# Kernel tuning notes

Measured on AMD Instinct MI355X. Metric: run time of the kernel, lower is better.

The kernel has to match this reference:

```python
import jax, jax.numpy as jnp
import numpy as np
from jax import lax

B, C, W = 16, 64, 125000  # batch, EEG channels, raw samples
KH, KW, SW, OC = 3, 2500, 1250, 32


def setup_inputs() -> dict:
    key = jax.random.key(0)
    ks = jax.random.split(key, 10)
    inp = {
        "x": jax.random.normal(ks[0], (B, 1, C, W), dtype=jnp.float32),
        # Conv2d(1->32, kernel=(3,2500))
        "conv_w": jax.random.normal(ks[1], (OC, 1, KH, KW), dtype=jnp.float32) * 0.02,
        "conv_b": jax.random.normal(ks[2], (OC,), dtype=jnp.float32) * 0.02,
        # Conv2d(32->1, kernel=(1,1))
        "conv2_w": jax.random.normal(ks[3], (1, OC, 1, 1), dtype=jnp.float32) * 0.1,
        "conv2_b": jax.random.normal(ks[4], (1,), dtype=jnp.float32) * 0.1,
        # nn.RNN(input_size=1, hidden_size=1): scalar weights
        "w_ih": jax.random.normal(ks[5], (1, 1), dtype=jnp.float32),
        "w_hh": jax.random.normal(ks[6], (1, 1), dtype=jnp.float32),
        "b_ih": jax.random.normal(ks[7], (1,), dtype=jnp.float32) * 0.1,
        "b_hh": jax.random.normal(ks[8], (1,), dtype=jnp.float32) * 0.1,
        # torch.rand(num_layers=1, B, 1) hidden init, reused for every row i
        "h0": jax.random.uniform(ks[9], (1, B, 1), dtype=jnp.float32),
    }
    return inp


def reference(x, conv_w, conv_b, conv2_w, conv2_b, w_ih, w_hh, b_ih, b_hh, h0):
    # F.pad(x, (0,0,1,1), 'replicate'): pad channel (height) dim by 1 each side
    xp = jnp.pad(x, ((0, 0), (0, 0), (1, 1), (0, 0)), mode="edge")
    # conv + relu -> [B, 32, C, T]
    y = lax.conv_general_dilated(
        xp, conv_w, window_strides=(1, SW), padding="VALID",
        dimension_numbers=("NCHW", "OIHW", "NCHW"))
    y = jax.nn.relu(y + conv_b[None, :, None, None])
    # 1x1 conv 32->1 + relu -> [B, C, T]
    z = jnp.einsum("bohw,o->bhw", y, conv2_w[0, :, 0, 0]) + conv2_b[0]
    z = jax.nn.relu(z)
    # Elman RNN with scalar weights, scanned over T; carry is [B, C]
    wih, whh = w_ih[0, 0], w_hh[0, 0]
    bias = b_ih[0] + b_hh[0]
    h_init = jnp.broadcast_to(h0[0, :, 0][:, None], z.shape[:2])  # [B, C]

    def step(h, xt):  # xt: [B, C]
        h = jnp.tanh(wih * xt + whh * h + bias)
        return h, None

    xs = jnp.moveaxis(z, -1, 0)  # [T, B, C]
    h_final, _ = lax.scan(step, h_init, xs)
    return jax.nn.sigmoid(h_final)  # [B, C]
```

## Files before the change

kernel.cpp:

```cpp
#include <hip/hip_runtime.h>
#include <math.h>

#define B_ 16
#define C_ 64
#define J_ 100
#define T_ 99
#define KW_ 1250
#define KP_ 1280
#define N_ 192
#define M_ (B_*C_*J_)
#define BM 128
#define BK 32
#define NCHUNK 40

typedef __attribute__((ext_vector_type(8))) _Float16 half8;
typedef __attribute__((ext_vector_type(4))) float f32x4;
typedef __attribute__((ext_vector_type(2), aligned(8))) float f32x2;

__global__ __launch_bounds__(256) void wconv_kernel(const float* __restrict__ cw,
                                                    _Float16* __restrict__ wh)
{
    int n = blockIdx.x;
    int o = n / 6, rem = n - o * 6, kh = rem >> 1, hf = rem & 1;
    const float* src = cw + o * 7500 + kh * 2500 + hf * 1250;
    for (int k = threadIdx.x; k < KP_; k += 256)
        wh[n * KP_ + k] = (k < KW_) ? (_Float16)src[k] : (_Float16)0.f;
}

__global__ __launch_bounds__(256, 3) void gemm_kernel(const float* __restrict__ x,
                                                      const _Float16* __restrict__ wh,
                                                      _Float16* __restrict__ P)
{
    __shared__ __align__(16) _Float16 smA[2][BM * BK];

    const int tid  = threadIdx.x;
    const int bm0  = blockIdx.x * BM;
    const int lane = tid & 63;
    const int wave = tid >> 6;
    const int wm   = (wave & 1) * 64;
    const int wn   = (wave >> 1) * 96;
    const int l15  = lane & 15;
    const int lq   = lane >> 4;

    const float* ap[2]; int koff[2]; int adst[2];
#pragma unroll
    for (int u = 0; u < 2; u++) {
        int q  = u * 256 + tid;
        int rl = q >> 2, p = q & 3;
        int gr = bm0 + rl;
        int b  = gr / 6400;
        int j  = (gr - b * 6400) >> 6;
        int c  = gr & 63;
        long xrow = (long)(b * 64 + c) * 100 + j;
        ap[u]   = x + xrow * KW_ + p * 8;
        koff[u] = p * 8;
        adst[u] = q * 8;
    }
    const _Float16* bbase = wh + (size_t)(wn + l15) * KP_ + lq * 8;

    f32x4 acc[4][6];
#pragma unroll
    for (int mi = 0; mi < 4; mi++)
#pragma unroll
        for (int ni = 0; ni < 6; ni++) acc[mi][ni] = (f32x4){0.f, 0.f, 0.f, 0.f};

    f32x2 areg[2][4];
#define LOADA(k0)                                                              \
    do {                                                                       \
        _Pragma("unroll") for (int u = 0; u < 2; u++)                          \
        _Pragma("unroll") for (int j2 = 0; j2 < 4; j2++) {                     \
            int k = (k0) + koff[u] + j2 * 2;           \
            areg[u][j2] = (k + 2 <= KW_)                                       \
                ? *(const f32x2*)(ap[u] + (k0) + j2 * 2)                       \
                : (f32x2){0.f, 0.f};                                           \
        }                                                                      \
    } while (0)

    LOADA(0);

    for (int ck = 0; ck < NCHUNK; ck++) {
        const int slot = ck & 1;
        _Float16* Ab = &smA[slot][0];

        half8 bcur = *(const half8*)(bbase + (size_t)ck * BK);

#pragma unroll
        for (int u = 0; u < 2; u++) {
            half8 h;
#pragma unroll
            for (int j2 = 0; j2 < 4; j2++) {
                h[2 * j2]     = (_Float16)areg[u][j2].x;
                h[2 * j2 + 1] = (_Float16)areg[u][j2].y;
            }
            *(half8*)(Ab + adst[u]) = h;
        }

        asm volatile("s_waitcnt lgkmcnt(0)" ::: "memory");
        __builtin_amdgcn_s_barrier();
        __builtin_amdgcn_sched_barrier(0);

        if (ck + 1 < NCHUNK) LOADA((ck + 1) * BK);

        half8 afr[4];
#pragma unroll
        for (int mi = 0; mi < 4; mi++)
            afr[mi] = *(const half8*)(Ab + (wm + mi * 16 + l15) * BK + lq * 8);

#pragma unroll
        for (int ni = 0; ni < 6; ni++) {
            half8 bnext = bcur;
            if (ni < 5)
                bnext = *(const half8*)(bbase + (size_t)(ni + 1) * 16 * KP_
                                              + (size_t)ck * BK);
#pragma unroll
            for (int mi = 0; mi < 4; mi++)
                acc[mi][ni] = __builtin_amdgcn_mfma_f32_16x16x32_f16(
                    afr[mi], bcur, acc[mi][ni], 0, 0, 0);
            bcur = bnext;
        }
    }

#pragma unroll
    for (int mi = 0; mi < 4; mi++) {
        int mrow = bm0 + wm + mi * 16 + lq * 4;
#pragma unroll
        for (int ni = 0; ni < 6; ni++) {
            int n = wn + ni * 16 + l15;
#pragma unroll
            for (int r2 = 0; r2 < 4; r2++)
                P[(size_t)(mrow + r2) * N_ + n] = (_Float16)acc[mi][ni][r2];
        }
    }
#undef LOADA
}

__global__ __launch_bounds__(256) void combine_kernel(const _Float16* __restrict__ P,
                                                      const float* __restrict__ conv_b,
                                                      const float* __restrict__ c2w,
                                                      const float* __restrict__ c2b,
                                                      float* __restrict__ z)
{
    __shared__ float Pl[64][193];
    __shared__ float red[4][64];
    const int t   = blockIdx.x;
    const int b   = blockIdx.y;
    const int tid = threadIdx.x;
    const int c   = tid & 63;
    const int og  = tid >> 6;

    float v[8];
#pragma unroll
    for (int o = 0; o < 8; o++) v[o] = conv_b[og * 8 + o];

    for (int hf = 0; hf < 2; hf++) {
        const int j = t + hf;
        const _Float16* Pb = P + (size_t)((b * 100 + j) * 64) * N_;
        __syncthreads();
#pragma unroll
        for (int i = 0; i < 6; i++) {
            int e   = i * 256 + tid;
            half8 h = *(const half8*)(Pb + e * 8);
            int row = e / 24;
            int col = (e - row * 24) * 8;
#pragma unroll
            for (int u = 0; u < 8; u++) Pl[row][col + u] = (float)h[u];
        }
        __syncthreads();
#pragma unroll
        for (int kh = 0; kh < 3; kh++) {
            int r = c + kh - 1;
            r = r < 0 ? 0 : (r > 63 ? 63 : r);
#pragma unroll
            for (int o = 0; o < 8; o++)
                v[o] += Pl[r][(og * 8 + o) * 6 + kh * 2 + hf];
        }
    }

    float part = 0.f;
#pragma unroll
    for (int o = 0; o < 8; o++) part += fmaxf(v[o], 0.f) * c2w[og * 8 + o];
    red[og][c] = part;
    __syncthreads();
    if (og == 0) {
        float zz = red[0][c] + red[1][c] + red[2][c] + red[3][c] + c2b[0];
        z[t * (B_ * C_) + b * 64 + c] = fmaxf(zz, 0.f);
    }
}

__global__ __launch_bounds__(256) void rnn_kernel(const float* __restrict__ z,
                                                  const float* __restrict__ w_ih,
                                                  const float* __restrict__ w_hh,
                                                  const float* __restrict__ b_ih,
                                                  const float* __restrict__ b_hh,
                                                  const float* __restrict__ h0,
                                                  float* __restrict__ out)
{
    __shared__ float zs[50][256];
    const int tid = threadIdx.x;
    const int g   = blockIdx.x * 256 + tid;
    const int b   = g >> 6;
    const float wih  = w_ih[0];
    const float whh  = w_hh[0];
    const float bias = b_ih[0] + b_hh[0];
    float h = h0[b];
    for (int t0 = 0; t0 < T_; t0 += 50) {
        const int nt = (T_ - t0) < 50 ? (T_ - t0) : 50;
        __syncthreads();
        for (int tt = 0; tt < nt; tt++)
            zs[tt][tid] = z[(t0 + tt) * (B_ * C_) + g];
        __syncthreads();
        for (int tt = 0; tt < nt; tt++)
            h = tanhf(fmaf(wih, zs[tt][tid], fmaf(whh, h, bias)));
    }
    out[g] = 1.f / (1.f + expf(-h));
}

extern "C" void kernel_launch(void* const* d_in, const int* in_sizes, int n_in,
                              void* d_out, int out_size, void* d_ws, size_t ws_size,
                              hipStream_t stream)
{
    const float* x   = (const float*)d_in[0];
    const float* cw  = (const float*)d_in[1];
    const float* cb  = (const float*)d_in[2];
    const float* c2w = (const float*)d_in[3];
    const float* c2b = (const float*)d_in[4];
    const float* wih = (const float*)d_in[5];
    const float* whh = (const float*)d_in[6];
    const float* bih = (const float*)d_in[7];
    const float* bhh = (const float*)d_in[8];
    const float* h0  = (const float*)d_in[9];
    float* out = (float*)d_out;

    const size_t whbytes = (size_t)N_ * KP_ * sizeof(_Float16);
    const size_t pbytes  = (size_t)M_ * N_ * sizeof(_Float16);
    const size_t zbytes  = (size_t)B_ * C_ * T_ * sizeof(float);

    if (ws_size < whbytes + pbytes + zbytes) return;

    _Float16* wh = (_Float16*)d_ws;
    _Float16* P  = (_Float16*)((char*)d_ws + whbytes);
    float*    z  = (float*)((char*)d_ws + whbytes + pbytes);

    wconv_kernel<<<N_, 256, 0, stream>>>(cw, wh);
    gemm_kernel<<<M_ / BM, 256, 0, stream>>>(x, wh, P);
    combine_kernel<<<dim3(T_, B_), 256, 0, stream>>>(P, cb, c2w, c2b, z);
    rnn_kernel<<<4, 256, 0, stream>>>(z, wih, whh, bih, bhh, h0, out);
}
```

Before: 860.0 us.

## Pre-pack A to fp16 tiles and stage GEMM via async global-to-LDS loads

Adds a pack kernel that converts the input x to fp16 and writes it in a chunk-tiled layout. The GEMM then streams A and B tiles into a triple-buffered LDS with global_load_lds and vmcnt-based waits, instead of converting floats in registers and reading B straight from global memory. The goal is to overlap memory with MFMA work and remove in-loop conversions and strided B loads. In exchange there is an extra pass over x (read fp32, write fp16 workspace), more LDS use per block, and occupancy lowered to 2.

New measurement: 841.5 us. 2.1% less time.

```diff
diff --git a/kernel.cpp b/kernel.cpp
--- a/kernel.cpp
+++ b/kernel.cpp
@@ -3,19 +3,23 @@
 
 #define B_ 16
 #define C_ 64
-#define J_ 100
 #define T_ 99
 #define KW_ 1250
 #define KP_ 1280
 #define N_ 192
-#define M_ (B_*C_*J_)
+#define M_ (B_*C_*100)
 #define BM 128
 #define BK 32
 #define NCHUNK 40
 
 typedef __attribute__((ext_vector_type(8))) _Float16 half8;
+typedef __attribute__((ext_vector_type(2))) _Float16 half2_t;
 typedef __attribute__((ext_vector_type(4))) float f32x4;
 typedef __attribute__((ext_vector_type(2), aligned(8))) float f32x2;
+
+#define GLD_LDS16(gp, lp) \
+    __builtin_amdgcn_global_load_lds((const __attribute__((address_space(1))) void*)(gp), \
+                                     (__attribute__((address_space(3))) void*)(lp), 16, 0, 0)
 
 __global__ __launch_bounds__(256) void wconv_kernel(const float* __restrict__ cw,
                                                     _Float16* __restrict__ wh)
@@ -27,36 +31,73 @@
         wh[n * KP_ + k] = (k < KW_) ? (_Float16)src[k] : (_Float16)0.f;
 }
 
-__global__ __launch_bounds__(256, 3) void gemm_kernel(const float* __restrict__ x,
+__global__ __launch_bounds__(256) void pack_kernel(const float* __restrict__ x,
+                                                   _Float16* __restrict__ Apk)
+{
+    __shared__ _Float16 As[16][1288];
+    const int g   = blockIdx.x;
+    const int tid = threadIdx.x;
+    const int i   = tid >> 4;
+    const int s   = tid & 15;
+    const int mrow = g * 16 + i;
+    const int b  = mrow / 6400;
+    const int jc = mrow - b * 6400;
+    const int j  = jc >> 6;
+    const int c  = jc & 63;
+    const float* xr = x + ((size_t)(b * 64 + c) * 100 + j) * KW_;
+
+#pragma unroll
+    for (int sw = 0; sw < 40; sw++) {
+        int t = s * 2 + sw * 32;
+        f32x2 v = (t + 2 <= KW_) ? *(const f32x2*)(xr + t) : (f32x2){0.f, 0.f};
+        *(half2_t*)(&As[i][t]) = (half2_t){(_Float16)v.x, (_Float16)v.y};
+    }
+    __syncthreads();
+
+    const int tile = g >> 3, ro = g & 7;
+#pragma unroll
+    for (int w = 0; w < 10; w++) {
+        int p  = tid + 256 * w;
+        int ck = p >> 6, rem = p & 63, ri = rem >> 2, kq = rem & 3;
+        half8 h = *(const half8*)(&As[ri][ck * 32 + kq * 8]);
+        *(half8*)(Apk + ((size_t)(tile * NCHUNK + ck) * 128 + ro * 16 + ri) * 32
+                      + kq * 8) = h;
+    }
+}
+
+__global__ __launch_bounds__(256, 2) void gemm_kernel(const _Float16* __restrict__ Apk,
                                                       const _Float16* __restrict__ wh,
                                                       _Float16* __restrict__ P)
 {
-    __shared__ __align__(16) _Float16 smA[2][BM * BK];
+    __shared__ __align__(16) _Float16 smA[3][BM * BK];
+    __shared__ __align__(16) _Float16 smB[3][N_ * BK];
 
     const int tid  = threadIdx.x;
-    const int bm0  = blockIdx.x * BM;
+    const int bt   = blockIdx.x;
     const int lane = tid & 63;
     const int wave = tid >> 6;
+    const int wq   = wave * 64;
     const int wm   = (wave & 1) * 64;
     const int wn   = (wave >> 1) * 96;
     const int l15  = lane & 15;
     const int lq   = lane >> 4;
 
-    const float* ap[2]; int koff[2]; int adst[2];
-#pragma unroll
-    for (int u = 0; u < 2; u++) {
-        int q  = u * 256 + tid;
-        int rl = q >> 2, p = q & 3;
-        int gr = bm0 + rl;
-        int b  = gr / 6400;
-        int j  = (gr - b * 6400) >> 6;
-        int c  = gr & 63;
-        long xrow = (long)(b * 64 + c) * 100 + j;
-        ap[u]   = x + xrow * KW_ + p * 8;
-        koff[u] = p * 8;
-        adst[u] = q * 8;
-    }
-    const _Float16* bbase = wh + (size_t)(wn + l15) * KP_ + lq * 8;
+    const _Float16* bp[3];
+#pragma unroll
+    for (int s = 0; s < 3; s++) {
+        int q = wq + 256 * s + lane;
+        bp[s] = wh + (size_t)(q >> 2) * KP_ + (q & 3) * 8;
+    }
+    const _Float16* abase = Apk + ((size_t)(bt * NCHUNK) << 12);
+
+#define STAGE(ck_, buf_) do {                                                    \
+        const _Float16* As_ = abase + ((size_t)(ck_) << 12);                     \
+        GLD_LDS16(As_ + (wq) * 8 + lane * 8,       &smA[buf_][(wq) * 8]);        \
+        GLD_LDS16(As_ + (wq + 256) * 8 + lane * 8, &smA[buf_][(wq + 256) * 8]);  \
+        GLD_LDS16(bp[0] + (size_t)(ck_) * BK,      &smB[buf_][(wq) * 8]);        \
+        GLD_LDS16(bp[1] + (size_t)(ck_) * BK,      &smB[buf_][(wq + 256) * 8]);  \
+        GLD_LDS16(bp[2] + (size_t)(ck_) * BK,      &smB[buf_][(wq + 512) * 8]);  \
+    } while (0)
 
     f32x4 acc[4][6];
 #pragma unroll
@@ -64,62 +105,45 @@
 #pragma unroll
         for (int ni = 0; ni < 6; ni++) acc[mi][ni] = (f32x4){0.f, 0.f, 0.f, 0.f};
 
-    f32x2 areg[2][4];
-#define LOADA(k0)                                                              \
-    do {                                                                       \
-        _Pragma("unroll") for (int u = 0; u < 2; u++)                          \
-        _Pragma("unroll") for (int j2 = 0; j2 < 4; j2++) {                     \
-            int k = (k0) + koff[u] + j2 * 2;           \
-            areg[u][j2] = (k + 2 <= KW_)                                       \
-                ? *(const f32x2*)(ap[u] + (k0) + j2 * 2)                       \
-                : (f32x2){0.f, 0.f};                                           \
-        }                                                                      \
-    } while (0)
-
-    LOADA(0);
-
+    STAGE(0, 0);
+    STAGE(1, 1);
+
+    int bi = 0;
     for (int ck = 0; ck < NCHUNK; ck++) {
-        const int slot = ck & 1;
-        _Float16* Ab = &smA[slot][0];
-
-        half8 bcur = *(const half8*)(bbase + (size_t)ck * BK);
-
-#pragma unroll
-        for (int u = 0; u < 2; u++) {
-            half8 h;
-#pragma unroll
-            for (int j2 = 0; j2 < 4; j2++) {
-                h[2 * j2]     = (_Float16)areg[u][j2].x;
-                h[2 * j2 + 1] = (_Float16)areg[u][j2].y;
-            }
-            *(half8*)(Ab + adst[u]) = h;
-        }
-
-        asm volatile("s_waitcnt lgkmcnt(0)" ::: "memory");
+        if (ck + 1 < NCHUNK) {
+            asm volatile("s_waitcnt vmcnt(5)" ::: "memory");
+        } else {
+            asm volatile("s_waitcnt vmcnt(0)" ::: "memory");
+        }
         __builtin_amdgcn_s_barrier();
         __builtin_amdgcn_sched_barrier(0);
 
-        if (ck + 1 < NCHUNK) LOADA((ck + 1) * BK);
-
-        half8 afr[4];
+        if (ck + 2 < NCHUNK) {
+            int b2 = bi + 2; if (b2 >= 3) b2 -= 3;
+            STAGE(ck + 2, b2);
+        }
+
+        const _Float16* Ab = &smA[bi][0];
+        const _Float16* Bb = &smB[bi][0];
+        half8 afr[4], bfr[6];
 #pragma unroll
         for (int mi = 0; mi < 4; mi++)
             afr[mi] = *(const half8*)(Ab + (wm + mi * 16 + l15) * BK + lq * 8);
-
-#pragma unroll
-        for (int ni = 0; ni < 6; ni++) {
-            half8 bnext = bcur;
-            if (ni < 5)
-                bnext = *(const half8*)(bbase + (size_t)(ni + 1) * 16 * KP_
-                                              + (size_t)ck * BK);
-#pragma unroll
-            for (int mi = 0; mi < 4; mi++)
+#pragma unroll
+        for (int ni = 0; ni < 6; ni++)
+            bfr[ni] = *(const half8*)(Bb + (wn + ni * 16 + l15) * BK + lq * 8);
+#pragma unroll
+        for (int mi = 0; mi < 4; mi++)
+#pragma unroll
+            for (int ni = 0; ni < 6; ni++)
                 acc[mi][ni] = __builtin_amdgcn_mfma_f32_16x16x32_f16(
-                    afr[mi], bcur, acc[mi][ni], 0, 0, 0);
-            bcur = bnext;
-        }
-    }
-
+                    afr[mi], bfr[ni], acc[mi][ni], 0, 0, 0);
+
+        bi = (bi == 2) ? 0 : bi + 1;
+    }
+#undef STAGE
+
+    const int bm0 = bt * BM;
 #pragma unroll
     for (int mi = 0; mi < 4; mi++) {
         int mrow = bm0 + wm + mi * 16 + lq * 4;
@@ -131,7 +155,6 @@
                 P[(size_t)(mrow + r2) * N_ + n] = (_Float16)acc[mi][ni][r2];
         }
     }
-#undef LOADA
 }
 
 __global__ __launch_bounds__(256) void combine_kernel(const _Float16* __restrict__ P,
@@ -231,18 +254,21 @@
     const float* h0  = (const float*)d_in[9];
     float* out = (float*)d_out;
 
-    const size_t whbytes = (size_t)N_ * KP_ * sizeof(_Float16);
-    const size_t pbytes  = (size_t)M_ * N_ * sizeof(_Float16);
-    const size_t zbytes  = (size_t)B_ * C_ * T_ * sizeof(float);
-
-    if (ws_size < whbytes + pbytes + zbytes) return;
-
-    _Float16* wh = (_Float16*)d_ws;
-    _Float16* P  = (_Float16*)((char*)d_ws + whbytes);
-    float*    z  = (float*)((char*)d_ws + whbytes + pbytes);
+    const size_t whbytes  = (size_t)N_ * KP_ * sizeof(_Float16);
+    const size_t apkbytes = (size_t)(M_ / BM) * NCHUNK * 4096 * sizeof(_Float16);
+    const size_t pbytes   = (size_t)M_ * N_ * sizeof(_Float16);
+    const size_t zbytes   = (size_t)B_ * C_ * T_ * sizeof(float);
+
+    if (ws_size < whbytes + apkbytes + pbytes + zbytes) return;
+
+    _Float16* wh  = (_Float16*)d_ws;
+    _Float16* Apk = (_Float16*)((char*)d_ws + whbytes);
+    _Float16* P   = (_Float16*)((char*)d_ws + whbytes + apkbytes);
+    float*    z   = (float*)((char*)d_ws + whbytes + apkbytes + pbytes);
 
     wconv_kernel<<<N_, 256, 0, stream>>>(cw, wh);
-    gemm_kernel<<<M_ / BM, 256, 0, stream>>>(x, wh, P);
+    pack_kernel<<<M_ / 16, 256, 0, stream>>>(x, Apk);
+    gemm_kernel<<<M_ / BM, 256, 0, stream>>>(Apk, wh, P);
     combine_kernel<<<dim3(T_, B_), 256, 0, stream>>>(P, cb, c2w, c2b, z);
     rnn_kernel<<<4, 256, 0, stream>>>(z, wih, whh, bih, bhh, h0, out);
 }
```

## Restructure GEMM A-tile staging into 128-wide K superchunks with coalesced row loads

Applied to the files above, without the earlier changes.

The GEMM now stages four BK chunks of the A operand at once. Each half-wave loads 16 full rows, with 32 lanes reading 2 floats each at two offsets, into a single padded LDS tile (stride 136). The old scheme spread each row over 4 threads in 32-element pieces. The aim is longer contiguous global reads, more loads in flight per stage, and fewer barriers per K element, with B fragments for all six N tiles loaded per 32-wide sub-chunk. In exchange, each thread holds 64 floats of A in registers and the occupancy hint drops from 3 to 2 blocks. There is also one LDS buffer with a trailing barrier instead of double buffering.

New measurement: 785.4 us. 1.09x faster.

```diff
diff --git a/kernel.cpp b/kernel.cpp
--- a/kernel.cpp
+++ b/kernel.cpp
@@ -3,17 +3,18 @@
 
 #define B_ 16
 #define C_ 64
-#define J_ 100
 #define T_ 99
 #define KW_ 1250
 #define KP_ 1280
 #define N_ 192
-#define M_ (B_*C_*J_)
+#define M_ (B_*C_*100)
 #define BM 128
 #define BK 32
-#define NCHUNK 40
+#define NSC 10
+#define ASTRIDE 136
 
 typedef __attribute__((ext_vector_type(8))) _Float16 half8;
+typedef __attribute__((ext_vector_type(2))) _Float16 half2_t;
 typedef __attribute__((ext_vector_type(4))) float f32x4;
 typedef __attribute__((ext_vector_type(2), aligned(8))) float f32x2;
 
@@ -27,14 +28,15 @@
         wh[n * KP_ + k] = (k < KW_) ? (_Float16)src[k] : (_Float16)0.f;
 }
 
-__global__ __launch_bounds__(256, 3) void gemm_kernel(const float* __restrict__ x,
+__global__ __launch_bounds__(256, 2) void gemm_kernel(const float* __restrict__ x,
                                                       const _Float16* __restrict__ wh,
                                                       _Float16* __restrict__ P)
 {
-    __shared__ __align__(16) _Float16 smA[2][BM * BK];
+    __shared__ __align__(16) _Float16 smA[BM * ASTRIDE];
 
     const int tid  = threadIdx.x;
-    const int bm0  = blockIdx.x * BM;
+    const int bt   = blockIdx.x;
+    const int bm0  = bt * BM;
     const int lane = tid & 63;
     const int wave = tid >> 6;
     const int wm   = (wave & 1) * 64;
@@ -42,20 +44,15 @@
     const int l15  = lane & 15;
     const int lq   = lane >> 4;
 
-    const float* ap[2]; int koff[2]; int adst[2];
-#pragma unroll
-    for (int u = 0; u < 2; u++) {
-        int q  = u * 256 + tid;
-        int rl = q >> 2, p = q & 3;
-        int gr = bm0 + rl;
-        int b  = gr / 6400;
-        int j  = (gr - b * 6400) >> 6;
-        int c  = gr & 63;
-        long xrow = (long)(b * 64 + c) * 100 + j;
-        ap[u]   = x + xrow * KW_ + p * 8;
-        koff[u] = p * 8;
-        adst[u] = q * 8;
-    }
+    const int h   = tid >> 5;
+    const int lw  = tid & 31;
+    const int lw2 = lw * 2;
+    const int rbase = h * 16;
+    const int bb   = bt / 50;
+    const int tloc = bt - bb * 50;
+    const long xrow0 = (long)(bb * 64 + (h & 3) * 16) * 100 + tloc * 2 + (h >> 2);
+    const float* apx = x + xrow0 * KW_ + lw2;
+
     const _Float16* bbase = wh + (size_t)(wn + l15) * KP_ + lq * 8;
 
     f32x4 acc[4][6];
@@ -64,61 +61,76 @@
 #pragma unroll
         for (int ni = 0; ni < 6; ni++) acc[mi][ni] = (f32x4){0.f, 0.f, 0.f, 0.f};
 
-    f32x2 areg[2][4];
-#define LOADA(k0)                                                              \
-    do {                                                                       \
-        _Pragma("unroll") for (int u = 0; u < 2; u++)                          \
-        _Pragma("unroll") for (int j2 = 0; j2 < 4; j2++) {                     \
-            int k = (k0) + koff[u] + j2 * 2;           \
-            areg[u][j2] = (k + 2 <= KW_)                                       \
-                ? *(const f32x2*)(ap[u] + (k0) + j2 * 2)                       \
-                : (f32x2){0.f, 0.f};                                           \
-        }                                                                      \
+    f32x2 areg[16][2];
+
+#define LOADA(sc_) do {                                                          \
+        const float* p_ = apx + (sc_) * 128;                                     \
+        if ((sc_) < NSC - 1) {                                                   \
+            _Pragma("unroll") for (int i = 0; i < 16; i++)                       \
+            _Pragma("unroll") for (int w = 0; w < 2; w++)                        \
+                areg[i][w] = *(const f32x2*)(p_ + (size_t)i * 125000 + w * 64);  \
+        } else {                                                                 \
+            _Pragma("unroll") for (int i = 0; i < 16; i++)                       \
+            _Pragma("unroll") for (int w = 0; w < 2; w++) {                      \
+                int k_ = (NSC - 1) * 128 + w * 64 + lw2;                         \
+                areg[i][w] = (k_ <= KW_ - 2)                                     \
+                    ? *(const f32x2*)(p_ + (size_t)i * 125000 + w * 64)          \
+                    : (f32x2){0.f, 0.f};                                         \
+            }                                                                    \
+        }                                                                        \
     } while (0)
 
     LOADA(0);
 
-    for (int ck = 0; ck < NCHUNK; ck++) {
-        const int slot = ck & 1;
-        _Float16* Ab = &smA[slot][0];
-
-        half8 bcur = *(const half8*)(bbase + (size_t)ck * BK);
-
-#pragma unroll
-        for (int u = 0; u < 2; u++) {
-            half8 h;
-#pragma unroll
-            for (int j2 = 0; j2 < 4; j2++) {
-                h[2 * j2]     = (_Float16)areg[u][j2].x;
-                h[2 * j2 + 1] = (_Float16)areg[u][j2].y;
+    for (int sc = 0; sc < NSC; sc++) {
+#pragma unroll
+        for (int i = 0; i < 16; i++) {
+            const int r = rbase + i;
+#pragma unroll
+            for (int w = 0; w < 2; w++) {
+                half2_t hh = {(_Float16)areg[i][w].x, (_Float16)areg[i][w].y};
+                *(half2_t*)(smA + r * ASTRIDE + w * 64 + lw2) = hh;
             }
-            *(half8*)(Ab + adst[u]) = h;
-        }
+        }
+
+        half8 bfr[6];
+#pragma unroll
+        for (int ni = 0; ni < 6; ni++)
+            bfr[ni] = *(const half8*)(bbase + (size_t)ni * 16 * KP_
+                                            + (size_t)(sc * 4) * BK);
 
         asm volatile("s_waitcnt lgkmcnt(0)" ::: "memory");
         __builtin_amdgcn_s_barrier();
         __builtin_amdgcn_sched_barrier(0);
 
-        if (ck + 1 < NCHUNK) LOADA((ck + 1) * BK);
-
-        half8 afr[4];
-#pragma unroll
-        for (int mi = 0; mi < 4; mi++)
-            afr[mi] = *(const half8*)(Ab + (wm + mi * 16 + l15) * BK + lq * 8);
-
-#pragma unroll
-        for (int ni = 0; ni < 6; ni++) {
-            half8 bnext = bcur;
-            if (ni < 5)
-                bnext = *(const half8*)(bbase + (size_t)(ni + 1) * 16 * KP_
-                                              + (size_t)ck * BK);
+        if (sc + 1 < NSC) LOADA(sc + 1);
+
+#pragma unroll
+        for (int ckl = 0; ckl < 4; ckl++) {
+            if (ckl > 0) {
+#pragma unroll
+                for (int ni = 0; ni < 6; ni++)
+                    bfr[ni] = *(const half8*)(bbase + (size_t)ni * 16 * KP_
+                                                    + (size_t)(sc * 4 + ckl) * BK);
+            }
+            half8 afr[4];
 #pragma unroll
             for (int mi = 0; mi < 4; mi++)
-                acc[mi][ni] = __builtin_amdgcn_mfma_f32_16x16x32_f16(
-                    afr[mi], bcur, acc[mi][ni], 0, 0, 0);
-            bcur = bnext;
-        }
-    }
+                afr[mi] = *(const half8*)(smA + (wm + mi * 16 + l15) * ASTRIDE
+                                              + ckl * 32 + lq * 8);
+#pragma unroll
+            for (int mi = 0; mi < 4; mi++)
+#pragma unroll
+                for (int ni = 0; ni < 6; ni++)
+                    acc[mi][ni] = __builtin_amdgcn_mfma_f32_16x16x32_f16(
+                        afr[mi], bfr[ni], acc[mi][ni], 0, 0, 0);
+        }
+
+        asm volatile("s_waitcnt lgkmcnt(0)" ::: "memory");
+        __builtin_amdgcn_s_barrier();
+        __builtin_amdgcn_sched_barrier(0);
+    }
+#undef LOADA
 
 #pragma unroll
     for (int mi = 0; mi < 4; mi++) {
@@ -131,7 +143,6 @@
                 P[(size_t)(mrow + r2) * N_ + n] = (_Float16)acc[mi][ni][r2];
         }
     }
-#undef LOADA
 }
 
 __global__ __launch_bounds__(256) void combine_kernel(const _Float16* __restrict__ P,
@@ -159,11 +170,11 @@
 #pragma unroll
         for (int i = 0; i < 6; i++) {
             int e   = i * 256 + tid;
-            half8 h = *(const half8*)(Pb + e * 8);
+            half8 hdat = *(const half8*)(Pb + e * 8);
             int row = e / 24;
             int col = (e - row * 24) * 8;
 #pragma unroll
-            for (int u = 0; u < 8; u++) Pl[row][col + u] = (float)h[u];
+            for (int u = 0; u < 8; u++) Pl[row][col + u] = (float)hdat[u];
         }
         __syncthreads();
 #pragma unroll
```
